# Performance work log

Hardware: AMD Instinct MI355X
Metric: run time of the kernel (lower is better)

## Reference

```python
import jax, jax.numpy as jnp
import numpy as np

N_NODES = 100000
N_EDGES = 3200000
F_IN = 128
F_HID = 16
F_OUT = 1


def setup_inputs() -> dict:
    key = jax.random.key(0)
    ks = jax.random.split(key, 8)
    x = jax.random.normal(ks[0], (N_NODES, F_IN), dtype=jnp.float32)
    src = jax.random.randint(ks[1], (N_EDGES,), 0, N_NODES, dtype=jnp.int32)
    dst = jax.random.randint(ks[2], (N_EDGES,), 0, N_NODES, dtype=jnp.int32)
    edge_w = jax.random.uniform(ks[3], (N_EDGES,), dtype=jnp.float32)
    W0 = jax.random.normal(ks[4], (F_IN, F_HID), dtype=jnp.float32) / np.sqrt(F_IN)
    b0 = jnp.zeros((F_HID,), dtype=jnp.float32)
    W1 = jax.random.normal(ks[5], (F_HID, F_OUT), dtype=jnp.float32) / np.sqrt(F_HID)
    b1 = jnp.zeros((F_OUT,), dtype=jnp.float32)
    return {"x": x, "src": src, "dst": dst, "edge_w": edge_w,
            "W0": W0, "b0": b0, "W1": W1, "b1": b1}


def _spmm(src, dst, edge_w, h):
    # sparse A (COO) @ dense h: gather rows at src, weight, scatter-add to dst
    msgs = h[src] * edge_w[:, None]            # [E, F]
    return jax.ops.segment_sum(msgs, dst, num_segments=N_NODES)  # [N, F]


def reference(x, src, dst, edge_w, W0, b0, W1, b1):
    # GCNConv layer 0: relu(A @ (x @ W0) + b0)
    z0 = x @ W0                                 # [N, 16] linear transform first
    h = jax.nn.relu(_spmm(src, dst, edge_w, z0) + b0)
    # (Dropout is identity at inference)
    # GCNConv layer 1: sigmoid(A @ (h @ W1) + b1)
    z1 = h @ W1                                 # [N, 1]
    out = jax.nn.sigmoid(_spmm(src, dst, edge_w, z1) + b1)
    return out
```

## Files before the change

### kernel.cpp

```cpp
#include <hip/hip_runtime.h>

#define N_NODES 100000
#define N_EDGES 3200000
#define F_IN 128
#define F_HID 16

#define BK_LG 8
#define BK_NODES 256
#define NB ((N_NODES + BK_NODES - 1) / BK_NODES)
#define NB_P 512
#define BCAP 9216
#define CHUNK 4096
#define BIN_T 512
#define EPT (CHUNK / BIN_T)
#define CUR_STRIDE 16

__device__ __forceinline__ unsigned short f2bf_rne(float f) {
    unsigned u = __float_as_uint(f);
    u += 0x7FFFu + ((u >> 16) & 1u);
    return (unsigned short)(u >> 16);
}

__global__ __launch_bounds__(256) void k_xw0(const float* __restrict__ x,
                                             const float* __restrict__ W0,
                                             unsigned short* __restrict__ z0b, int n) {
    __shared__ float xs[64][F_IN + 1];
    __shared__ float w0s[F_IN * F_HID];
    const int tid = threadIdx.x;
    for (int i = tid; i < F_IN * F_HID; i += 256) w0s[i] = W0[i];
    const int row0 = blockIdx.x * 64;
    for (int i = tid; i < 64 * (F_IN / 4); i += 256) {
        int r  = i / (F_IN / 4);
        int c4 = i % (F_IN / 4);
        float4 v = make_float4(0.f, 0.f, 0.f, 0.f);
        int row = row0 + r;
        if (row < n) v = ((const float4*)(x + (size_t)row * F_IN))[c4];
        xs[r][c4 * 4 + 0] = v.x; xs[r][c4 * 4 + 1] = v.y;
        xs[r][c4 * 4 + 2] = v.z; xs[r][c4 * 4 + 3] = v.w;
    }
    __syncthreads();
    const int r  = tid & 63;
    const int cg = tid >> 6;
    float a0 = 0.f, a1 = 0.f, a2 = 0.f, a3 = 0.f;
    #pragma unroll 8
    for (int k = 0; k < F_IN; ++k) {
        float xv = xs[r][k];
        a0 = fmaf(xv, w0s[k * F_HID + cg * 4 + 0], a0);
        a1 = fmaf(xv, w0s[k * F_HID + cg * 4 + 1], a1);
        a2 = fmaf(xv, w0s[k * F_HID + cg * 4 + 2], a2);
        a3 = fmaf(xv, w0s[k * F_HID + cg * 4 + 3], a3);
    }
    int row = row0 + r;
    if (row < n) {
        ushort4 p = make_ushort4(f2bf_rne(a0), f2bf_rne(a1), f2bf_rne(a2), f2bf_rne(a3));
        *(ushort4*)(z0b + (size_t)row * F_HID + cg * 4) = p;
    }
}

__global__ __launch_bounds__(BIN_T) void k_bin(const int* __restrict__ src,
                                               const int* __restrict__ dst,
                                               const float* __restrict__ ew,
                                               int* __restrict__ gcursor,
                                               int2* __restrict__ ebin) {
    __shared__ int cnt[NB_P], scn[NB_P], run[NB_P], gb[NB_P], alw[NB_P];
    __shared__ int2 stage[CHUNK];
    __shared__ unsigned short sbid[CHUNK];
    const int tid = threadIdx.x;
    const int e0  = blockIdx.x * CHUNK;
    const int nch = min(CHUNK, N_EDGES - e0);

    for (int i = tid; i < NB_P; i += BIN_T) cnt[i] = 0;
    __syncthreads();

    int es[EPT], eb[EPT], edl[EPT]; float ww[EPT];
    #pragma unroll
    for (int k = 0; k < EPT; ++k) {
        int idx = k * BIN_T + tid;
        if (idx < nch) {
            int e = e0 + idx;
            int d = dst[e];
            es[k]  = src[e];
            ww[k]  = ew[e];
            eb[k]  = d >> BK_LG;
            edl[k] = d & (BK_NODES - 1);
            atomicAdd(&cnt[eb[k]], 1);
        } else {
            eb[k] = -1;
        }
    }
    __syncthreads();

    scn[tid] = cnt[tid];
    __syncthreads();
    for (int off = 1; off < NB_P; off <<= 1) {
        int v = 0;
        if (tid >= off) v = scn[tid - off];
        __syncthreads();
        if (tid >= off) scn[tid] += v;
        __syncthreads();
    }

    if (tid < NB) {
        int c = cnt[tid];
        if (c > 0) {
            int old = atomicAdd(&gcursor[tid * CUR_STRIDE], c);
            int a = BCAP - old;
            a = (a < 0) ? 0 : ((a > c) ? c : a);
            alw[tid] = a;
            gb[tid]  = tid * BCAP + old;
        } else {
            alw[tid] = 0;
            gb[tid]  = tid * BCAP;
        }
        run[tid] = 0;
    }
    __syncthreads();

    #pragma unroll
    for (int k = 0; k < EPT; ++k) {
        if (eb[k] >= 0) {
            int b = eb[k];
            int p = (scn[b] - cnt[b]) + atomicAdd(&run[b], 1);
            stage[p] = make_int2(__float_as_int(ww[k]), es[k] | (edl[k] << 17));
            sbid[p]  = (unsigned short)b;
        }
    }
    __syncthreads();

    for (int s = tid; s < nch; s += BIN_T) {
        int b   = sbid[s];
        int off = s - (scn[b] - cnt[b]);
        if (off < alw[b]) ebin[(size_t)gb[b] + off] = stage[s];
    }
}

__global__ __launch_bounds__(512) void k_sort(const int* __restrict__ gcursor,
                                              const int2* __restrict__ ebin,
                                              int2* __restrict__ ebin2,
                                              int2* __restrict__ rowinfo) {
    __shared__ int hist[BK_NODES], excl[BK_NODES], run[BK_NODES], tmp[BK_NODES];
    const int tid = threadIdx.x;
    const int b   = blockIdx.x;
    if (tid < BK_NODES) hist[tid] = 0;
    __syncthreads();
    const int   ecnt = min(gcursor[b * CUR_STRIDE], BCAP);
    const int2* eb   = ebin + (size_t)b * BCAP;
    for (int i = tid; i < ecnt; i += 512) {
        atomicAdd(&hist[eb[i].y >> 17], 1);
    }
    __syncthreads();
    if (tid < BK_NODES) tmp[tid] = hist[tid];
    __syncthreads();
    for (int off = 1; off < BK_NODES; off <<= 1) {
        int v = 0;
        if (tid < BK_NODES && tid >= off) v = tmp[tid - off];
        __syncthreads();
        if (tid < BK_NODES && tid >= off) tmp[tid] += v;
        __syncthreads();
    }
    if (tid < BK_NODES) {
        excl[tid] = tmp[tid] - hist[tid];
        run[tid]  = 0;
        int v = b * BK_NODES + tid;
        if (v < N_NODES)
            rowinfo[v] = make_int2(b * BCAP + excl[tid], hist[tid]);
    }
    __syncthreads();
    int2* ob = ebin2 + (size_t)b * BCAP;
    for (int i = tid; i < ecnt; i += 512) {
        int2 e = eb[i];
        int dl = e.y >> 17;
        int p  = excl[dl] + atomicAdd(&run[dl], 1);
        ob[p] = e;
    }
}

__global__ __launch_bounds__(256) void k_gather0(const int2* __restrict__ rowinfo,
                                                 const int2* __restrict__ ebin2,
                                                 const unsigned short* __restrict__ z0b,
                                                 const float* __restrict__ b0,
                                                 const float* __restrict__ W1,
                                                 float* __restrict__ z1) {
    const int tid  = threadIdx.x;
    const int lane = tid & 63;
    const int f2   = lane & 7;
    const int g    = lane >> 3;
    const int v    = blockIdx.x * 4 + (tid >> 6);
    if (v >= N_NODES) return;
    const int2 ri = rowinfo[v];
    const int2* sl = ebin2 + ri.x;
    const int dv = ri.y;
    float acc0 = 0.f, acc1 = 0.f;
    const int2 zed = make_int2(0, 0);
    for (int j = g; j < dv; j += 16) {
        int2 e0 = sl[j];
        int2 e1 = (j + 8 < dv) ? sl[j + 8] : zed;
        unsigned u0 = *(const unsigned*)(z0b + (size_t)(e0.y & 0x1FFFF) * F_HID + f2 * 2);
        unsigned u1 = *(const unsigned*)(z0b + (size_t)(e1.y & 0x1FFFF) * F_HID + f2 * 2);
        float w0 = __int_as_float(e0.x), w1 = __int_as_float(e1.x);
        acc0 = fmaf(__uint_as_float(u0 << 16),          w0, acc0);
        acc1 = fmaf(__uint_as_float(u0 & 0xFFFF0000u),  w0, acc1);
        acc0 = fmaf(__uint_as_float(u1 << 16),          w1, acc0);
        acc1 = fmaf(__uint_as_float(u1 & 0xFFFF0000u),  w1, acc1);
    }
    acc0 += __shfl_xor(acc0, 8);  acc1 += __shfl_xor(acc1, 8);
    acc0 += __shfl_xor(acc0, 16); acc1 += __shfl_xor(acc1, 16);
    acc0 += __shfl_xor(acc0, 32); acc1 += __shfl_xor(acc1, 32);
    float2 bb = *(const float2*)(b0 + f2 * 2);
    float2 wv = *(const float2*)(W1 + f2 * 2);
    float c = fmaxf(acc0 + bb.x, 0.f) * wv.x + fmaxf(acc1 + bb.y, 0.f) * wv.y;
    c += __shfl_xor(c, 1);
    c += __shfl_xor(c, 2);
    c += __shfl_xor(c, 4);
    if (lane == 0) z1[v] = c;
}

__global__ __launch_bounds__(256) void k_gather1(const int2* __restrict__ rowinfo,
                                                 const int2* __restrict__ ebin2,
                                                 const float* __restrict__ z1,
                                                 const float* __restrict__ b1,
                                                 float* __restrict__ out) {
    const int tid = threadIdx.x;
    const int l8  = tid & 7;
    const int v   = blockIdx.x * 32 + (tid >> 3);
    if (v >= N_NODES) return;
    const int2 ri = rowinfo[v];
    const int2* sl = ebin2 + ri.x;
    const int dv = ri.y;
    float acc = 0.f;
    const int2 zed = make_int2(0, 0);
    for (int j = l8; j < dv; j += 16) {
        int2 e0 = sl[j];
        int2 e1 = (j + 8 < dv) ? sl[j + 8] : zed;
        acc = fmaf(z1[e0.y & 0x1FFFF], __int_as_float(e0.x), acc);
        acc = fmaf(z1[e1.y & 0x1FFFF], __int_as_float(e1.x), acc);
    }
    #pragma unroll
    for (int off = 1; off < 8; off <<= 1) acc += __shfl_xor(acc, off);
    if (l8 == 0) {
        float t = acc + b1[0];
        out[v] = 1.f / (1.f + expf(-t));
    }
}

extern "C" void kernel_launch(void* const* d_in, const int* in_sizes, int n_in,
                              void* d_out, int out_size, void* d_ws, size_t ws_size,
                              hipStream_t stream) {
    const float* x   = (const float*)d_in[0];
    const int*   src = (const int*)d_in[1];
    const int*   dst = (const int*)d_in[2];
    const float* ew  = (const float*)d_in[3];
    const float* W0  = (const float*)d_in[4];
    const float* b0  = (const float*)d_in[5];
    const float* W1  = (const float*)d_in[6];
    const float* b1  = (const float*)d_in[7];
    float* out = (float*)d_out;

    unsigned short* z0b = (unsigned short*)d_ws;
    float* z1      = (float*)(z0b + (size_t)N_NODES * F_HID);
    int*   gcursor = (int*)(z1 + N_NODES);
    int2*  rowinfo = (int2*)(gcursor + NB * CUR_STRIDE);
    int2*  ebin    = rowinfo + (size_t)NB * BK_NODES;
    int2*  ebin2   = ebin + (size_t)NB * BCAP;

    hipMemsetAsync(gcursor, 0, (size_t)NB * CUR_STRIDE * sizeof(int), stream);

    k_bin    <<<(N_EDGES + CHUNK - 1) / CHUNK, BIN_T, 0, stream>>>(src, dst, ew,
                                                                   gcursor, ebin);
    k_xw0    <<<(N_NODES + 63) / 64, 256, 0, stream>>>(x, W0, z0b, N_NODES);
    k_sort   <<<NB, 512, 0, stream>>>(gcursor, ebin, ebin2, rowinfo);
    k_gather0<<<(N_NODES + 3) / 4,   256, 0, stream>>>(rowinfo, ebin2, z0b, b0, W1, z1);
    k_gather1<<<(N_NODES + 31) / 32, 256, 0, stream>>>(rowinfo, ebin2, z1, b1, out);
}
```

Baseline: 153.2 us.

## Fuse x@W0 with edge binning, widen buckets and use shuffle scans

Merges the dense x@W0 kernel and the edge-binning kernel into one launch, with even blocks doing the matmul and odd blocks binning an edge chunk, so the two independent stages overlap on the GPU. Doubles the bucket width to 512 nodes, halves the bin chunk to 2048 edges, and replaces the barrier-heavy Hillis-Steele scans in binning and sorting with wavefront shuffle scans. It also rounds x to bf16 in shared memory before the matmul, which halves LDS use but adds rounding error on the input features. Larger buckets mean fewer, bigger sort blocks, which changes the sort's parallelism and its shared-memory atomic contention.

```diff
diff --git a/kernel.cpp b/kernel.cpp
--- a/kernel.cpp
+++ b/kernel.cpp
@@ -5,14 +5,13 @@
 #define F_IN 128
 #define F_HID 16
 
-#define BK_LG 8
-#define BK_NODES 256
-#define NB ((N_NODES + BK_NODES - 1) / BK_NODES)
-#define NB_P 512
-#define BCAP 9216
-#define CHUNK 4096
-#define BIN_T 512
-#define EPT (CHUNK / BIN_T)
+#define BK_LG 9
+#define BK_NODES 512
+#define NBK ((N_NODES + BK_NODES - 1) / BK_NODES)
+#define NBK_P 256
+#define BCAP 17664
+#define CH1 2048
+#define NCH1 ((N_EDGES + CH1 - 1) / CH1)
 #define CUR_STRIDE 16
 
 __device__ __forceinline__ unsigned short f2bf_rne(float f) {
@@ -21,217 +20,237 @@
     return (unsigned short)(u >> 16);
 }
 
-__global__ __launch_bounds__(256) void k_xw0(const float* __restrict__ x,
+__global__ __launch_bounds__(256) void k_pre(const float* __restrict__ x,
                                              const float* __restrict__ W0,
-                                             unsigned short* __restrict__ z0b, int n) {
-    __shared__ float xs[64][F_IN + 1];
-    __shared__ float w0s[F_IN * F_HID];
+                                             unsigned short* __restrict__ z0b,
+                                             const int* __restrict__ src,
+                                             const int* __restrict__ dst,
+                                             const float* __restrict__ ew,
+                                             int* __restrict__ cursorC,
+                                             int2* __restrict__ ebinC) {
+    __shared__ __align__(16) char smem[24832];
     const int tid = threadIdx.x;
-    for (int i = tid; i < F_IN * F_HID; i += 256) w0s[i] = W0[i];
-    const int row0 = blockIdx.x * 64;
-    for (int i = tid; i < 64 * (F_IN / 4); i += 256) {
-        int r  = i / (F_IN / 4);
-        int c4 = i % (F_IN / 4);
-        float4 v = make_float4(0.f, 0.f, 0.f, 0.f);
+
+    if ((blockIdx.x & 1) == 0) {
+        const int xb = blockIdx.x >> 1;
+        unsigned short* xsb = (unsigned short*)smem;
+        float* w0s = (float*)(smem + 16640);
+        for (int i = tid; i < F_IN * F_HID; i += 256) w0s[i] = W0[i];
+        const int row0 = xb * 64;
+        for (int i = tid; i < 64 * 32; i += 256) {
+            int r = i >> 5, c4 = i & 31;
+            float4 v = make_float4(0.f, 0.f, 0.f, 0.f);
+            int row = row0 + r;
+            if (row < N_NODES) v = ((const float4*)(x + (size_t)row * F_IN))[c4];
+            *(ushort2*)(xsb + r * 130 + c4 * 4)     = make_ushort2(f2bf_rne(v.x), f2bf_rne(v.y));
+            *(ushort2*)(xsb + r * 130 + c4 * 4 + 2) = make_ushort2(f2bf_rne(v.z), f2bf_rne(v.w));
+        }
+        __syncthreads();
+        const int r  = tid & 63;
+        const int cg = tid >> 6;
+        float a0 = 0.f, a1 = 0.f, a2 = 0.f, a3 = 0.f;
+        #pragma unroll 4
+        for (int k = 0; k < F_IN; k += 2) {
+            unsigned u = *(const unsigned*)(xsb + r * 130 + k);
+            float xv0 = __uint_as_float(u << 16);
+            float xv1 = __uint_as_float(u & 0xFFFF0000u);
+            const float* wr0 = w0s + k * F_HID + cg * 4;
+            const float* wr1 = wr0 + F_HID;
+            a0 = fmaf(xv0, wr0[0], a0); a1 = fmaf(xv0, wr0[1], a1);
+            a2 = fmaf(xv0, wr0[2], a2); a3 = fmaf(xv0, wr0[3], a3);
+            a0 = fmaf(xv1, wr1[0], a0); a1 = fmaf(xv1, wr1[1], a1);
+            a2 = fmaf(xv1, wr1[2], a2); a3 = fmaf(xv1, wr1[3], a3);
+        }
         int row = row0 + r;
-        if (row < n) v = ((const float4*)(x + (size_t)row * F_IN))[c4];
-        xs[r][c4 * 4 + 0] = v.x; xs[r][c4 * 4 + 1] = v.y;
-        xs[r][c4 * 4 + 2] = v.z; xs[r][c4 * 4 + 3] = v.w;
-    }
-    __syncthreads();
-    const int r  = tid & 63;
-    const int cg = tid >> 6;
-    float a0 = 0.f, a1 = 0.f, a2 = 0.f, a3 = 0.f;
-    #pragma unroll 8
-    for (int k = 0; k < F_IN; ++k) {
-        float xv = xs[r][k];
-        a0 = fmaf(xv, w0s[k * F_HID + cg * 4 + 0], a0);
-        a1 = fmaf(xv, w0s[k * F_HID + cg * 4 + 1], a1);
-        a2 = fmaf(xv, w0s[k * F_HID + cg * 4 + 2], a2);
-        a3 = fmaf(xv, w0s[k * F_HID + cg * 4 + 3], a3);
-    }
-    int row = row0 + r;
-    if (row < n) {
-        ushort4 p = make_ushort4(f2bf_rne(a0), f2bf_rne(a1), f2bf_rne(a2), f2bf_rne(a3));
-        *(ushort4*)(z0b + (size_t)row * F_HID + cg * 4) = p;
-    }
-}
-
-__global__ __launch_bounds__(BIN_T) void k_bin(const int* __restrict__ src,
-                                               const int* __restrict__ dst,
-                                               const float* __restrict__ ew,
-                                               int* __restrict__ gcursor,
-                                               int2* __restrict__ ebin) {
-    __shared__ int cnt[NB_P], scn[NB_P], run[NB_P], gb[NB_P], alw[NB_P];
-    __shared__ int2 stage[CHUNK];
-    __shared__ unsigned short sbid[CHUNK];
-    const int tid = threadIdx.x;
-    const int e0  = blockIdx.x * CHUNK;
-    const int nch = min(CHUNK, N_EDGES - e0);
-
-    for (int i = tid; i < NB_P; i += BIN_T) cnt[i] = 0;
-    __syncthreads();
-
-    int es[EPT], eb[EPT], edl[EPT]; float ww[EPT];
+        if (row < N_NODES) {
+            ushort4 p = make_ushort4(f2bf_rne(a0), f2bf_rne(a1),
+                                     f2bf_rne(a2), f2bf_rne(a3));
+            *(ushort4*)(z0b + (size_t)row * F_HID + cg * 4) = p;
+        }
+    } else {
+        const int ch = blockIdx.x >> 1;
+        int2* stage = (int2*)smem;
+        unsigned char* sbid = (unsigned char*)(smem + 16384);
+        int* cnt  = (int*)(smem + 18432);
+        int* excl = (int*)(smem + 19456);
+        int* run  = (int*)(smem + 20480);
+        int* gb   = (int*)(smem + 21504);
+        int* alw  = (int*)(smem + 22528);
+        int* wtot = (int*)(smem + 23552);
+        const int e0  = ch * CH1;
+        const int nch = min(CH1, N_EDGES - e0);
+
+        cnt[tid] = 0;
+        __syncthreads();
+
+        int es[8], eb[8], edl[8]; float ww[8];
+        #pragma unroll
+        for (int k = 0; k < 8; ++k) {
+            int idx = k * 256 + tid;
+            if (idx < nch) {
+                int e = e0 + idx;
+                int d = dst[e];
+                es[k]  = src[e];
+                ww[k]  = ew[e];
+                eb[k]  = d >> BK_LG;
+                edl[k] = d & (BK_NODES - 1);
+                atomicAdd(&cnt[eb[k]], 1);
+            } else {
+                eb[k] = -1;
+            }
+        }
+        __syncthreads();
+
+        {
+            const int lane = tid & 63, wid = tid >> 6;
+            int c_ = cnt[tid], inc = c_;
+            #pragma unroll
+            for (int off = 1; off < 64; off <<= 1) {
+                int t = __shfl_up(inc, off);
+                if (lane >= off) inc += t;
+            }
+            if (lane == 63) wtot[wid] = inc;
+            __syncthreads();
+            int base = 0;
+            #pragma unroll
+            for (int w = 0; w < 4; ++w) base += (w < wid) ? wtot[w] : 0;
+            excl[tid] = base + inc - c_;
+        }
+        __syncthreads();
+
+        if (tid < NBK) {
+            int c = cnt[tid];
+            if (c > 0) {
+                int old = atomicAdd(&cursorC[tid * CUR_STRIDE], c);
+                int a = BCAP - old;
+                a = (a < 0) ? 0 : ((a > c) ? c : a);
+                alw[tid] = a;
+                gb[tid]  = tid * BCAP + old;
+            } else {
+                alw[tid] = 0;
+                gb[tid]  = tid * BCAP;
+            }
+            run[tid] = 0;
+        }
+        __syncthreads();
+
+        #pragma unroll
+        for (int k = 0; k < 8; ++k) {
+            if (eb[k] >= 0) {
+                int b = eb[k];
+                int p = excl[b] + atomicAdd(&run[b], 1);
+                stage[p] = make_int2(__float_as_int(ww[k]), es[k] | (edl[k] << 17));
+                sbid[p]  = (unsigned char)b;
+            }
+        }
+        __syncthreads();
+
+        for (int s = tid; s < nch; s += 256) {
+            int b   = sbid[s];
+            int off = s - excl[b];
+            if (off < alw[b]) ebinC[(size_t)gb[b] + off] = stage[s];
+        }
+    }
+}
+
+__global__ __launch_bounds__(512) void k_sort2(const int* __restrict__ cursorC,
+                                               const int2* __restrict__ ebinC,
+                                               int2* __restrict__ sortedC,
+                                               int2* __restrict__ rowinfo) {
+    __shared__ int dcnt[BK_NODES], excl[BK_NODES], run[BK_NODES];
+    __shared__ int wtot[8];
+    const int tid = threadIdx.x, lane = tid & 63, wid = tid >> 6;
+    const int c = blockIdx.x;
+    dcnt[tid] = 0; run[tid] = 0;
+    __syncthreads();
+    const int   ecnt = min(cursorC[c * CUR_STRIDE], BCAP);
+    const int2* eC   = ebinC + (size_t)c * BCAP;
+    for (int i = tid; i < ecnt; i += 512) atomicAdd(&dcnt[eC[i].y >> 17], 1);
+    __syncthreads();
+    int d_ = dcnt[tid], inc = d_;
     #pragma unroll
-    for (int k = 0; k < EPT; ++k) {
-        int idx = k * BIN_T + tid;
-        if (idx < nch) {
-            int e = e0 + idx;
-            int d = dst[e];
-            es[k]  = src[e];
-            ww[k]  = ew[e];
-            eb[k]  = d >> BK_LG;
-            edl[k] = d & (BK_NODES - 1);
-            atomicAdd(&cnt[eb[k]], 1);
-        } else {
-            eb[k] = -1;
-        }
-    }
-    __syncthreads();
-
-    scn[tid] = cnt[tid];
-    __syncthreads();
-    for (int off = 1; off < NB_P; off <<= 1) {
-        int v = 0;
-        if (tid >= off) v = scn[tid - off];
-        __syncthreads();
-        if (tid >= off) scn[tid] += v;
-        __syncthreads();
-    }
-
-    if (tid < NB) {
-        int c = cnt[tid];
-        if (c > 0) {
-            int old = atomicAdd(&gcursor[tid * CUR_STRIDE], c);
-            int a = BCAP - old;
-            a = (a < 0) ? 0 : ((a > c) ? c : a);
-            alw[tid] = a;
-            gb[tid]  = tid * BCAP + old;
-        } else {
-            alw[tid] = 0;
-            gb[tid]  = tid * BCAP;
-        }
-        run[tid] = 0;
-    }
-    __syncthreads();
-
+    for (int off = 1; off < 64; off <<= 1) {
+        int t = __shfl_up(inc, off);
+        if (lane >= off) inc += t;
+    }
+    if (lane == 63) wtot[wid] = inc;
+    __syncthreads();
+    int base = 0;
     #pragma unroll
-    for (int k = 0; k < EPT; ++k) {
-        if (eb[k] >= 0) {
-            int b = eb[k];
-            int p = (scn[b] - cnt[b]) + atomicAdd(&run[b], 1);
-            stage[p] = make_int2(__float_as_int(ww[k]), es[k] | (edl[k] << 17));
-            sbid[p]  = (unsigned short)b;
-        }
-    }
-    __syncthreads();
-
-    for (int s = tid; s < nch; s += BIN_T) {
-        int b   = sbid[s];
-        int off = s - (scn[b] - cnt[b]);
-        if (off < alw[b]) ebin[(size_t)gb[b] + off] = stage[s];
-    }
-}
-
-__global__ __launch_bounds__(512) void k_sort(const int* __restrict__ gcursor,
-                                              const int2* __restrict__ ebin,
-                                              int2* __restrict__ ebin2,
-                                              int2* __restrict__ rowinfo) {
-    __shared__ int hist[BK_NODES], excl[BK_NODES], run[BK_NODES], tmp[BK_NODES];
-    const int tid = threadIdx.x;
-    const int b   = blockIdx.x;
-    if (tid < BK_NODES) hist[tid] = 0;
-    __syncthreads();
-    const int   ecnt = min(gcursor[b * CUR_STRIDE], BCAP);
-    const int2* eb   = ebin + (size_t)b * BCAP;
+    for (int w = 0; w < 8; ++w) base += (w < wid) ? wtot[w] : 0;
+    int ex = base + inc - d_;
+    excl[tid] = ex;
+    int v = c * BK_NODES + tid;
+    if (v < N_NODES) rowinfo[v] = make_int2(c * BCAP + ex, d_);
+    __syncthreads();
+    int2* oB = sortedC + (size_t)c * BCAP;
     for (int i = tid; i < ecnt; i += 512) {
-        atomicAdd(&hist[eb[i].y >> 17], 1);
-    }
-    __syncthreads();
-    if (tid < BK_NODES) tmp[tid] = hist[tid];
-    __syncthreads();
-    for (int off = 1; off < BK_NODES; off <<= 1) {
-        int v = 0;
-        if (tid < BK_NODES && tid >= off) v = tmp[tid - off];
-        __syncthreads();
-        if (tid < BK_NODES && tid >= off) tmp[tid] += v;
-        __syncthreads();
-    }
-    if (tid < BK_NODES) {
-        excl[tid] = tmp[tid] - hist[tid];
-        run[tid]  = 0;
-        int v = b * BK_NODES + tid;
-        if (v < N_NODES)
-            rowinfo[v] = make_int2(b * BCAP + excl[tid], hist[tid]);
-    }
-    __syncthreads();
-    int2* ob = ebin2 + (size_t)b * BCAP;
-    for (int i = tid; i < ecnt; i += 512) {
-        int2 e = eb[i];
+        int2 e = eC[i];
         int dl = e.y >> 17;
         int p  = excl[dl] + atomicAdd(&run[dl], 1);
-        ob[p] = e;
-    }
-}
-
-__global__ __launch_bounds__(256) void k_gather0(const int2* __restrict__ rowinfo,
-                                                 const int2* __restrict__ ebin2,
-                                                 const unsigned short* __restrict__ z0b,
-                                                 const float* __restrict__ b0,
-                                                 const float* __restrict__ W1,
-                                                 float* __restrict__ z1) {
-    const int tid  = threadIdx.x;
+        oB[p] = e;
+    }
+}
+
+__global__ __launch_bounds__(256) void k_g0(const int2* __restrict__ rowinfo,
+                                            const int2* __restrict__ sortedC,
+                                            const unsigned short* __restrict__ z0b,
+                                            const float* __restrict__ b0,
+                                            const float* __restrict__ W1,
+                                            float* __restrict__ z1) {
+    __shared__ float b0s[16], w1s[16];
+    const int tid = threadIdx.x;
+    if (tid < 16) { b0s[tid] = b0[tid]; w1s[tid] = W1[tid]; }
+    __syncthreads();
     const int lane = tid & 63;
+    const int v    = blockIdx.x * 4 + (tid >> 6);
+    if (v >= N_NODES) return;
+    const int2 ri  = rowinfo[v];
+    const int2* sl = sortedC + ri.x;
+    const int dv   = ri.y;
     const int f2   = lane & 7;
     const int g    = lane >> 3;
-    const int v    = blockIdx.x * 4 + (tid >> 6);
-    if (v >= N_NODES) return;
-    const int2 ri = rowinfo[v];
-    const int2* sl = ebin2 + ri.x;
-    const int dv = ri.y;
     float acc0 = 0.f, acc1 = 0.f;
-    const int2 zed = make_int2(0, 0);
     for (int j = g; j < dv; j += 16) {
         int2 e0 = sl[j];
-        int2 e1 = (j + 8 < dv) ? sl[j + 8] : zed;
+        int  j1 = j + 8;
+        int2 e1 = (j1 < dv) ? sl[j1] : make_int2(0, 0);
         unsigned u0 = *(const unsigned*)(z0b + (size_t)(e0.y & 0x1FFFF) * F_HID + f2 * 2);
         unsigned u1 = *(const unsigned*)(z0b + (size_t)(e1.y & 0x1FFFF) * F_HID + f2 * 2);
         float w0 = __int_as_float(e0.x), w1 = __int_as_float(e1.x);
-        acc0 = fmaf(__uint_as_float(u0 << 16),          w0, acc0);
-        acc1 = fmaf(__uint_as_float(u0 & 0xFFFF0000u),  w0, acc1);
-        acc0 = fmaf(__uint_as_float(u1 << 16),          w1, acc0);
-        acc1 = fmaf(__uint_as_float(u1 & 0xFFFF0000u),  w1, acc1);
+        acc0 = fmaf(__uint_as_float(u0 << 16),         w0, acc0);
+        acc1 = fmaf(__uint_as_float(u0 & 0xFFFF0000u), w0, acc1);
+        acc0 = fmaf(__uint_as_float(u1 << 16),         w1, acc0);
+        acc1 = fmaf(__uint_as_float(u1 & 0xFFFF0000u), w1, acc1);
     }
     acc0 += __shfl_xor(acc0, 8);  acc1 += __shfl_xor(acc1, 8);
     acc0 += __shfl_xor(acc0, 16); acc1 += __shfl_xor(acc1, 16);
     acc0 += __shfl_xor(acc0, 32); acc1 += __shfl_xor(acc1, 32);
-    float2 bb = *(const float2*)(b0 + f2 * 2);
-    float2 wv = *(const float2*)(W1 + f2 * 2);
-    float c = fmaxf(acc0 + bb.x, 0.f) * wv.x + fmaxf(acc1 + bb.y, 0.f) * wv.y;
-    c += __shfl_xor(c, 1);
-    c += __shfl_xor(c, 2);
-    c += __shfl_xor(c, 4);
-    if (lane == 0) z1[v] = c;
-}
-
-__global__ __launch_bounds__(256) void k_gather1(const int2* __restrict__ rowinfo,
-                                                 const int2* __restrict__ ebin2,
-                                                 const float* __restrict__ z1,
-                                                 const float* __restrict__ b1,
-                                                 float* __restrict__ out) {
+    float cc = fmaxf(acc0 + b0s[f2 * 2], 0.f) * w1s[f2 * 2]
+             + fmaxf(acc1 + b0s[f2 * 2 + 1], 0.f) * w1s[f2 * 2 + 1];
+    cc += __shfl_xor(cc, 1);
+    cc += __shfl_xor(cc, 2);
+    cc += __shfl_xor(cc, 4);
+    if (lane == 0) z1[v] = cc;
+}
+
+__global__ __launch_bounds__(256) void k_g1(const int2* __restrict__ rowinfo,
+                                            const int2* __restrict__ sortedC,
+                                            const float* __restrict__ z1,
+                                            const float* __restrict__ b1,
+                                            float* __restrict__ out) {
     const int tid = threadIdx.x;
     const int l8  = tid & 7;
     const int v   = blockIdx.x * 32 + (tid >> 3);
     if (v >= N_NODES) return;
-    const int2 ri = rowinfo[v];
-    const int2* sl = ebin2 + ri.x;
-    const int dv = ri.y;
+    const int2 ri  = rowinfo[v];
+    const int2* sl = sortedC + ri.x;
+    const int dv   = ri.y;
     float acc = 0.f;
-    const int2 zed = make_int2(0, 0);
     for (int j = l8; j < dv; j += 16) {
         int2 e0 = sl[j];
-        int2 e1 = (j + 8 < dv) ? sl[j + 8] : zed;
+        int  j1 = j + 8;
+        int2 e1 = (j1 < dv) ? sl[j1] : make_int2(0, 0);
         acc = fmaf(z1[e0.y & 0x1FFFF], __int_as_float(e0.x), acc);
         acc = fmaf(z1[e1.y & 0x1FFFF], __int_as_float(e1.x), acc);
     }
@@ -258,17 +277,15 @@
 
     unsigned short* z0b = (unsigned short*)d_ws;
     float* z1      = (float*)(z0b + (size_t)N_NODES * F_HID);
-    int*   gcursor = (int*)(z1 + N_NODES);
-    int2*  rowinfo = (int2*)(gcursor + NB * CUR_STRIDE);
-    int2*  ebin    = rowinfo + (size_t)NB * BK_NODES;
-    int2*  ebin2   = ebin + (size_t)NB * BCAP;
-
-    hipMemsetAsync(gcursor, 0, (size_t)NB * CUR_STRIDE * sizeof(int), stream);
-
-    k_bin    <<<(N_EDGES + CHUNK - 1) / CHUNK, BIN_T, 0, stream>>>(src, dst, ew,
-                                                                   gcursor, ebin);
-    k_xw0    <<<(N_NODES + 63) / 64, 256, 0, stream>>>(x, W0, z0b, N_NODES);
-    k_sort   <<<NB, 512, 0, stream>>>(gcursor, ebin, ebin2, rowinfo);
-    k_gather0<<<(N_NODES + 3) / 4,   256, 0, stream>>>(rowinfo, ebin2, z0b, b0, W1, z1);
-    k_gather1<<<(N_NODES + 31) / 32, 256, 0, stream>>>(rowinfo, ebin2, z1, b1, out);
-}
+    int*   cursorC = (int*)(z1 + N_NODES);
+    int2*  rowinfo = (int2*)(cursorC + NBK * CUR_STRIDE);
+    int2*  ebinC   = rowinfo + N_NODES;
+    int2*  sortedC = ebinC + (size_t)NBK * BCAP;
+
+    hipMemsetAsync(cursorC, 0, (size_t)NBK * CUR_STRIDE * sizeof(int), stream);
+
+    k_pre  <<<2 * NCH1, 256, 0, stream>>>(x, W0, z0b, src, dst, ew, cursorC, ebinC);
+    k_sort2<<<NBK, 512, 0, stream>>>(cursorC, ebinC, sortedC, rowinfo);
+    k_g0   <<<(N_NODES + 3) / 4,   256, 0, stream>>>(rowinfo, sortedC, z0b, b0, W1, z1);
+    k_g1   <<<(N_NODES + 31) / 32, 256, 0, stream>>>(rowinfo, sortedC, z1, b1, out);
+}
```

Result: no change. 151.4 us (-1.2%).
